# Performance work log

Measured on AMD Instinct MI355X. Metric: run time of the kernel, lower is better.

The kernel has to match this reference:

```python
import jax, jax.numpy as jnp
import numpy as np

LN_EPS = 1e-5
BN_EPS = 1e-5
HEADS = 8
KERNEL = 31
GROUP_SIZE = 8  # depthwise_conv groups = inner_dim // 8


def _ln(x, g, b):
    mu = jnp.mean(x, axis=-1, keepdims=True)
    var = jnp.var(x, axis=-1, keepdims=True)
    return (x - mu) * jax.lax.rsqrt(var + LN_EPS) * g + b


def _ff(x, g, b, w_in, b_in, w_out, b_out):
    h = _ln(x, g, b)
    y = h @ w_in.T + b_in
    a, c = jnp.split(y, 2, axis=-1)
    return (jax.nn.silu(a) * c) @ w_out.T + b_out


def _attn(x, g, b, wqkv, bqkv, wo, bo):
    B, S, _ = x.shape
    h = _ln(x, g, b)
    qkv = (h @ wqkv.T + bqkv).reshape(B, S, 3, HEADS, -1).transpose(2, 0, 3, 1, 4)
    q, k, v = qkv[0], qkv[1], qkv[2]  # [B,H,S,D]
    scale = q.shape[-1] ** -0.5
    scores = jnp.einsum('bhqd,bhkd->bhqk', q, k) * scale
    w = jax.nn.softmax(scores, axis=-1)
    o = jnp.einsum('bhqk,bhkd->bhqd', w, v)
    o = o.transpose(0, 2, 1, 3).reshape(B, S, -1)
    return o @ wo.T + bo


def _conv(x, g, b, pw1_w, pw1_b, dw_w, dw_b, bn_g, bn_b, bn_m, bn_v, pw2_w, pw2_b):
    h = _ln(x, g, b).transpose(0, 2, 1)  # [B, C, S]
    y = jnp.einsum('oc,bcs->bos', pw1_w[:, :, 0], h) + pw1_b[:, None]
    a, c = jnp.split(y, 2, axis=1)
    y = a * jax.nn.sigmoid(c)  # GLU over channel dim -> [B, inner, S]
    pad = (KERNEL - 1) // 2
    groups = y.shape[1] // dw_w.shape[1]  # inner_dim // 8
    y = jax.lax.conv_general_dilated(
        y, dw_w, window_strides=(1,), padding=[(pad, pad)],
        dimension_numbers=('NCH', 'OIH', 'NCH'), feature_group_count=groups)
    y = y + dw_b[:, None]
    y = (y - bn_m[:, None]) * jax.lax.rsqrt(bn_v[:, None] + BN_EPS) * bn_g[:, None] + bn_b[:, None]
    y = jax.nn.silu(y)
    y = jnp.einsum('oc,bcs->bos', pw2_w[:, :, 0], y) + pw2_b[:, None]
    return y.transpose(0, 2, 1)


def setup_inputs() -> dict:
    key = jax.random.key(0)
    dim, mult, exp = 512, 4, 2
    inner = dim * exp  # 1024
    ks = jax.random.split(key, 16)
    n = lambda k, shp: (jax.random.normal(k, shp, dtype=jnp.float32) * 0.02)
    d = {}
    d['x'] = jax.random.normal(ks[0], (8, 1024, dim), dtype=jnp.float32)
    # ff1
    d['ff1_g'] = jnp.ones((dim,), jnp.float32); d['ff1_b'] = jnp.zeros((dim,), jnp.float32)
    d['ff1_win'] = n(ks[1], (dim * mult * 2, dim)); d['ff1_bin'] = jnp.zeros((dim * mult * 2,), jnp.float32)
    d['ff1_wout'] = n(ks[2], (dim, dim * mult)); d['ff1_bout'] = jnp.zeros((dim,), jnp.float32)
    # attn
    d['attn_g'] = jnp.ones((dim,), jnp.float32); d['attn_b'] = jnp.zeros((dim,), jnp.float32)
    d['wqkv'] = n(ks[3], (3 * dim, dim)); d['bqkv'] = jnp.zeros((3 * dim,), jnp.float32)
    d['wo'] = n(ks[4], (dim, dim)); d['bo'] = jnp.zeros((dim,), jnp.float32)
    # conv
    d['conv_g'] = jnp.ones((dim,), jnp.float32); d['conv_b'] = jnp.zeros((dim,), jnp.float32)
    d['pw1_w'] = n(ks[5], (inner * 2, dim, 1)); d['pw1_b'] = jnp.zeros((inner * 2,), jnp.float32)
    d['dw_w'] = n(ks[6], (inner, GROUP_SIZE, KERNEL)); d['dw_b'] = jnp.zeros((inner,), jnp.float32)
    d['bn_g'] = jnp.ones((inner,), jnp.float32); d['bn_b'] = jnp.zeros((inner,), jnp.float32)
    d['bn_m'] = jnp.zeros((inner,), jnp.float32); d['bn_v'] = jnp.ones((inner,), jnp.float32)
    d['pw2_w'] = n(ks[7], (dim, inner, 1)); d['pw2_b'] = jnp.zeros((dim,), jnp.float32)
    # ff2
    d['ff2_g'] = jnp.ones((dim,), jnp.float32); d['ff2_b'] = jnp.zeros((dim,), jnp.float32)
    d['ff2_win'] = n(ks[8], (dim * mult * 2, dim)); d['ff2_bin'] = jnp.zeros((dim * mult * 2,), jnp.float32)
    d['ff2_wout'] = n(ks[9], (dim, dim * mult)); d['ff2_bout'] = jnp.zeros((dim,), jnp.float32)
    # final norm
    d['fn_g'] = jnp.ones((dim,), jnp.float32); d['fn_b'] = jnp.zeros((dim,), jnp.float32)
    return d


def reference(x, ff1_g, ff1_b, ff1_win, ff1_bin, ff1_wout, ff1_bout,
              attn_g, attn_b, wqkv, bqkv, wo, bo,
              conv_g, conv_b, pw1_w, pw1_b, dw_w, dw_b, bn_g, bn_b, bn_m, bn_v, pw2_w, pw2_b,
              ff2_g, ff2_b, ff2_win, ff2_bin, ff2_wout, ff2_bout, fn_g, fn_b):
    x = x + 0.5 * _ff(x, ff1_g, ff1_b, ff1_win, ff1_bin, ff1_wout, ff1_bout)
    x = x + _attn(x, attn_g, attn_b, wqkv, bqkv, wo, bo)
    x = x + _conv(x, conv_g, conv_b, pw1_w, pw1_b, dw_w, dw_b, bn_g, bn_b, bn_m, bn_v, pw2_w, pw2_b)
    x = x + 0.5 * _ff(x, ff2_g, ff2_b, ff2_win, ff2_bin, ff2_wout, ff2_bout)
    return _ln(x, fn_g, fn_b)
```

## Files before the change

kernel.cpp:

```cpp
#include <hip/hip_runtime.h>

#define SEQ   1024
#define BATCH 8
#define DIM   512
#define NTOK  (SEQ * BATCH)

typedef unsigned short ushort_t;
typedef unsigned int uint_t;
typedef __attribute__((ext_vector_type(8))) short s16x8;
typedef __attribute__((ext_vector_type(4))) float f32x4;

union F4 { float4 v; float f[4]; };

__device__ __forceinline__ float sigmoid_f(float x) { return 1.0f / (1.0f + expf(-x)); }
__device__ __forceinline__ float silu_f(float x)    { return x * sigmoid_f(x); }

__device__ __forceinline__ ushort_t f2bf(float x) {
  uint_t u = __float_as_uint(x);
  return (ushort_t)((u + 0x7FFFu + ((u >> 16) & 1u)) >> 16);
}
__device__ __forceinline__ float bf2f(ushort_t h) {
  return __uint_as_float(((uint_t)h) << 16);
}

__device__ __forceinline__ void gload16(const void* g, void* l) {
  __builtin_amdgcn_global_load_lds(
      (const __attribute__((address_space(1))) void*)g,
      (__attribute__((address_space(3))) void*)l,
      16, 0, 0);
}

struct CastArgs {
  const float* src[8];
  ushort_t*    dst[8];
  int          cum8[8];
};

__global__ __launch_bounds__(256) void f2b_multi(CastArgs a, int total8)
{
  const int i = blockIdx.x * 256 + threadIdx.x;
  if (i >= total8) return;
  int s = 0;
  #pragma unroll
  for (int k = 1; k < 8; ++k) s += (i >= a.cum8[k]) ? 1 : 0;
  const int j = i - a.cum8[s];
  const float* src = a.src[s] + (size_t)j * 8;
  F4 x0, x1;
  x0.v = *(const float4*)(src);
  x1.v = *(const float4*)(src + 4);
  uint4 o;
  o.x = (uint_t)f2bf(x0.f[0]) | ((uint_t)f2bf(x0.f[1]) << 16);
  o.y = (uint_t)f2bf(x0.f[2]) | ((uint_t)f2bf(x0.f[3]) << 16);
  o.z = (uint_t)f2bf(x1.f[0]) | ((uint_t)f2bf(x1.f[1]) << 16);
  o.w = (uint_t)f2bf(x1.f[2]) | ((uint_t)f2bf(x1.f[3]) << 16);
  *(uint4*)(a.dst[s] + (size_t)j * 8) = o;
}

template <int BF>
__global__ __launch_bounds__(256) void ln512_kernel(
    const float* __restrict__ in, const float* __restrict__ g,
    const float* __restrict__ b, void* __restrict__ outv)
{
  const int row = blockIdx.x * 4 + (threadIdx.x >> 6);
  const int l   = threadIdx.x & 63;
  const float* rp = in + (size_t)row * DIM + l * 8;
  F4 v0, v1;
  v0.v = *(const float4*)(rp);
  v1.v = *(const float4*)(rp + 4);
  float sum = 0.f, sq = 0.f;
  #pragma unroll
  for (int j = 0; j < 4; ++j) { sum += v0.f[j] + v1.f[j];
                                sq  += v0.f[j]*v0.f[j] + v1.f[j]*v1.f[j]; }
  #pragma unroll
  for (int m = 32; m >= 1; m >>= 1) {
    sum += __shfl_xor(sum, m, 64);
    sq  += __shfl_xor(sq,  m, 64);
  }
  const float mu   = sum * (1.0f / DIM);
  const float var  = sq * (1.0f / DIM) - mu * mu;
  const float rinv = rsqrtf(var + 1e-5f);
  F4 g0, g1, b0, b1;
  g0.v = *(const float4*)(g + l * 8);     g1.v = *(const float4*)(g + l * 8 + 4);
  b0.v = *(const float4*)(b + l * 8);     b1.v = *(const float4*)(b + l * 8 + 4);
  float o[8];
  #pragma unroll
  for (int j = 0; j < 4; ++j) {
    o[j]     = (v0.f[j] - mu) * rinv * g0.f[j] + b0.f[j];
    o[4 + j] = (v1.f[j] - mu) * rinv * g1.f[j] + b1.f[j];
  }
  if (BF) {
    uint4 u;
    u.x = (uint_t)f2bf(o[0]) | ((uint_t)f2bf(o[1]) << 16);
    u.y = (uint_t)f2bf(o[2]) | ((uint_t)f2bf(o[3]) << 16);
    u.z = (uint_t)f2bf(o[4]) | ((uint_t)f2bf(o[5]) << 16);
    u.w = (uint_t)f2bf(o[6]) | ((uint_t)f2bf(o[7]) << 16);
    *(uint4*)((ushort_t*)outv + (size_t)row * DIM + l * 8) = u;
  } else {
    F4 w0, w1;
    #pragma unroll
    for (int j = 0; j < 4; ++j) { w0.f[j] = o[j]; w1.f[j] = o[4 + j]; }
    *(float4*)((float*)outv + (size_t)row * DIM + l * 8)     = w0.v;
    *(float4*)((float*)outv + (size_t)row * DIM + l * 8 + 4) = w1.v;
  }
}

template <int EPI>
__global__ __launch_bounds__(256) void gemm_bf16(
    const ushort_t* __restrict__ A, const ushort_t* __restrict__ W,
    const float* __restrict__ bias, float* __restrict__ out,
    int N, int K, const float* __restrict__ res, float alpha)
{
  __shared__ ushort_t As[128 * 32];
  __shared__ ushort_t Ws[128 * 32];
  const int t    = threadIdx.x;
  const int lane = t & 63;
  const int w    = t >> 6;
  const int wm   = w >> 1, wn = w & 1;
  const int m0   = blockIdx.y << 7, n0 = blockIdx.x << 7;

  f32x4 acc[4][4] = {};

  const int lds0 = __builtin_amdgcn_readfirstlane((w * 64) * 16);
  const int lds1 = __builtin_amdgcn_readfirstlane((256 + w * 64) * 16);
  const int r0c  = t >> 2;
  const int r1c  = 64 + (t >> 2);
  const int cc   = (t & 3) << 3;

  for (int k0 = 0; k0 < K; k0 += 32) {
    gload16(A + (size_t)(m0 + r0c) * K + k0 + cc, (char*)As + lds0);
    gload16(A + (size_t)(m0 + r1c) * K + k0 + cc, (char*)As + lds1);
    gload16(W + (size_t)(n0 + r0c) * K + k0 + cc, (char*)Ws + lds0);
    gload16(W + (size_t)(n0 + r1c) * K + k0 + cc, (char*)Ws + lds1);
    __syncthreads();
    s16x8 a[4], b[4];
    #pragma unroll
    for (int i = 0; i < 4; ++i)
      a[i] = *(const s16x8*)&As[(wm * 64 + i * 16 + (lane & 15)) * 32 + ((lane >> 4) << 3)];
    #pragma unroll
    for (int j = 0; j < 4; ++j)
      b[j] = *(const s16x8*)&Ws[(wn * 64 + j * 16 + (lane & 15)) * 32 + ((lane >> 4) << 3)];
    #pragma unroll
    for (int i = 0; i < 4; ++i)
      #pragma unroll
      for (int j = 0; j < 4; ++j)
        acc[i][j] = __builtin_amdgcn_mfma_f32_16x16x32_bf16(a[i], b[j], acc[i][j], 0, 0, 0);
    __syncthreads();
  }

  #pragma unroll
  for (int i = 0; i < 4; ++i) {
    #pragma unroll
    for (int j = 0; j < 4; ++j) {
      const int col  = n0 + wn * 64 + j * 16 + (lane & 15);
      const int rowb = m0 + wm * 64 + i * 16 + ((lane >> 4) << 2);
      const float bc = bias[col];
      #pragma unroll
      for (int r = 0; r < 4; ++r) {
        const size_t idx = (size_t)(rowb + r) * N + col;
        float v = acc[i][j][r] + bc;
        if (EPI == 1) v = res[idx] + alpha * v;
        out[idx] = v;
      }
    }
  }
}

__global__ __launch_bounds__(256) void gemm_qkv_bf16(
    const ushort_t* __restrict__ A, const ushort_t* __restrict__ W,
    const float* __restrict__ bias, ushort_t* __restrict__ qkvb,
    ushort_t* __restrict__ Vt, int K)
{
  const int N = 1536;
  __shared__ ushort_t As[128 * 32];
  __shared__ ushort_t Ws[128 * 32];
  const int t    = threadIdx.x;
  const int lane = t & 63;
  const int w    = t >> 6;
  const int wm   = w >> 1, wn = w & 1;
  const int m0   = blockIdx.y << 7, n0 = blockIdx.x << 7;

  f32x4 acc[4][4] = {};

  const int lds0 = __builtin_amdgcn_readfirstlane((w * 64) * 16);
  const int lds1 = __builtin_amdgcn_readfirstlane((256 + w * 64) * 16);
  const int r0c  = t >> 2;
  const int r1c  = 64 + (t >> 2);
  const int cc   = (t & 3) << 3;

  for (int k0 = 0; k0 < K; k0 += 32) {
    gload16(A + (size_t)(m0 + r0c) * K + k0 + cc, (char*)As + lds0);
    gload16(A + (size_t)(m0 + r1c) * K + k0 + cc, (char*)As + lds1);
    gload16(W + (size_t)(n0 + r0c) * K + k0 + cc, (char*)Ws + lds0);
    gload16(W + (size_t)(n0 + r1c) * K + k0 + cc, (char*)Ws + lds1);
    __syncthreads();
    s16x8 a[4], b[4];
    #pragma unroll
    for (int i = 0; i < 4; ++i)
      a[i] = *(const s16x8*)&As[(wm * 64 + i * 16 + (lane & 15)) * 32 + ((lane >> 4) << 3)];
    #pragma unroll
    for (int j = 0; j < 4; ++j)
      b[j] = *(const s16x8*)&Ws[(wn * 64 + j * 16 + (lane & 15)) * 32 + ((lane >> 4) << 3)];
    #pragma unroll
    for (int i = 0; i < 4; ++i)
      #pragma unroll
      for (int j = 0; j < 4; ++j)
        acc[i][j] = __builtin_amdgcn_mfma_f32_16x16x32_bf16(a[i], b[j], acc[i][j], 0, 0, 0);
    __syncthreads();
  }

  #pragma unroll
  for (int i = 0; i < 4; ++i) {
    #pragma unroll
    for (int j = 0; j < 4; ++j) {
      const int col  = n0 + wn * 64 + j * 16 + (lane & 15);
      const int rowb = m0 + wm * 64 + i * 16 + ((lane >> 4) << 2);
      const float bc = bias[col];
      if (col < 1024) {
        #pragma unroll
        for (int r = 0; r < 4; ++r)
          qkvb[(size_t)(rowb + r) * N + col] = f2bf(acc[i][j][r] + bc);
      } else {
        const int vc = col - 1024;
        const int hh = vc >> 6, d = vc & 63;
        const int bb = rowb >> 10, s = rowb & 1023;
        ushort4 o;
        o.x = f2bf(acc[i][j][0] + bc);
        o.y = f2bf(acc[i][j][1] + bc);
        o.z = f2bf(acc[i][j][2] + bc);
        o.w = f2bf(acc[i][j][3] + bc);
        *(ushort4*)&Vt[(size_t)((bb * 8 + hh) * 64 + d) * 1024 + s] = o;
      }
    }
  }
}

template <int CGLU>
__global__ __launch_bounds__(256) void gemm_glu_bf16(
    const ushort_t* __restrict__ A, const ushort_t* __restrict__ W,
    const float* __restrict__ bias, ushort_t* __restrict__ out,
    int NG, int K)
{
  __shared__ ushort_t As[128 * 32];
  __shared__ ushort_t Was[64 * 32];
  __shared__ ushort_t Wcs[64 * 32];
  const int t    = threadIdx.x;
  const int lane = t & 63;
  const int w    = t >> 6;
  const int wm   = w >> 1, wn = w & 1;
  const int m0   = blockIdx.y << 7, n0 = blockIdx.x << 6;

  f32x4 acca[4][2] = {};
  f32x4 accc[4][2] = {};

  const int lds0 = __builtin_amdgcn_readfirstlane((w * 64) * 16);
  const int lds1 = __builtin_amdgcn_readfirstlane((256 + w * 64) * 16);
  const int r0c  = t >> 2;
  const int r1c  = 64 + (t >> 2);
  const int cc   = (t & 3) << 3;

  const ushort_t* Wc = W + (size_t)NG * K;

  for (int k0 = 0; k0 < K; k0 += 32) {
    gload16(A  + (size_t)(m0 + r0c) * K + k0 + cc, (char*)As  + lds0);
    gload16(A  + (size_t)(m0 + r1c) * K + k0 + cc, (char*)As  + lds1);
    gload16(W  + (size_t)(n0 + r0c) * K + k0 + cc, (char*)Was + lds0);
    gload16(Wc + (size_t)(n0 + r0c) * K + k0 + cc, (char*)Wcs + lds0);
    __syncthreads();
    s16x8 a[4], ba[2], bc[2];
    #pragma unroll
    for (int i = 0; i < 4; ++i)
      a[i] = *(const s16x8*)&As[(wm * 64 + i * 16 + (lane & 15)) * 32 + ((lane >> 4) << 3)];
    #pragma unroll
    for (int j = 0; j < 2; ++j) {
      const int roff = (wn * 32 + j * 16 + (lane & 15)) * 32 + ((lane >> 4) << 3);
      ba[j] = *(const s16x8*)&Was[roff];
      bc[j] = *(const s16x8*)&Wcs[roff];
    }
    #pragma unroll
    for (int i = 0; i < 4; ++i)
      #pragma unroll
      for (int j = 0; j < 2; ++j) {
        acca[i][j] = __builtin_amdgcn_mfma_f32_16x16x32_bf16(a[i], ba[j], acca[i][j], 0, 0, 0);
        accc[i][j] = __builtin_amdgcn_mfma_f32_16x16x32_bf16(a[i], bc[j], accc[i][j], 0, 0, 0);
      }
    __syncthreads();
  }

  #pragma unroll
  for (int i = 0; i < 4; ++i) {
    #pragma unroll
    for (int j = 0; j < 2; ++j) {
      const int col  = n0 + wn * 32 + j * 16 + (lane & 15);
      const int rowb = m0 + wm * 64 + i * 16 + ((lane >> 4) << 2);
      const float b1 = bias[col];
      const float b2 = bias[NG + col];
      #pragma unroll
      for (int r = 0; r < 4; ++r) {
        const float av = acca[i][j][r] + b1;
        const float cv = accc[i][j][r] + b2;
        const float o  = CGLU ? (av * sigmoid_f(cv)) : (silu_f(av) * cv);
        out[(size_t)(rowb + r) * NG + col] = f2bf(o);
      }
    }
  }
}

__global__ __launch_bounds__(256) void attn_mfma(
    const ushort_t* __restrict__ qkv, const ushort_t* __restrict__ Vt,
    ushort_t* __restrict__ out)
{
  __shared__ ushort_t Ks[64 * 64];
  __shared__ ushort_t Vs[64 * 64];
  __shared__ ushort_t Ps[4][16 * 64];

  const int t    = threadIdx.x;
  const int lane = t & 63;
  const int w    = t >> 6;
  const int i    = lane & 15;
  const int g    = lane >> 4;
  const int bh   = blockIdx.x;
  const int b    = bh >> 3, h = bh & 7;
  const int qt   = blockIdx.y;

  s16x8 qf[2];
  {
    const ushort_t* qrow = qkv + (size_t)(b * SEQ + qt * 64 + w * 16 + i) * 1536 + h * 64;
    qf[0] = *(const s16x8*)(qrow + g * 8);
    qf[1] = *(const s16x8*)(qrow + 32 + g * 8);
  }

  float m_[4], l_[4];
  f32x4 po[4] = {};
  #pragma unroll
  for (int r = 0; r < 4; ++r) { m_[r] = -1e30f; l_[r] = 0.0f; }

  const int e0   = w * 2;
  const int off0 = __builtin_amdgcn_readfirstlane(e0 * 1024);
  const int off1 = __builtin_amdgcn_readfirstlane(e0 * 1024 + 1024);

  for (int kvt = 0; kvt < 16; ++kvt) {
    __syncthreads();
    {
      const int s_a = e0 * 64 + lane;
      const int ra = s_a >> 3, ca = (s_a & 7) ^ (ra & 7);
      const int s_b = s_a + 64;
      const int rb = s_b >> 3, cb2 = (s_b & 7) ^ (rb & 7);
      gload16(qkv + (size_t)(b * SEQ + kvt * 64 + ra) * 1536 + 512 + h * 64 + ca * 8,
              (char*)Ks + off0);
      gload16(qkv + (size_t)(b * SEQ + kvt * 64 + rb) * 1536 + 512 + h * 64 + cb2 * 8,
              (char*)Ks + off1);
      gload16(Vt + (size_t)(bh * 64 + ra) * SEQ + kvt * 64 + ca * 8,
              (char*)Vs + off0);
      gload16(Vt + (size_t)(bh * 64 + rb) * SEQ + kvt * 64 + cb2 * 8,
              (char*)Vs + off1);
    }
    __syncthreads();

    f32x4 sc[4] = {};
    #pragma unroll
    for (int jj = 0; jj < 4; ++jj) {
      const int row = jj * 16 + i;
      #pragma unroll
      for (int dd = 0; dd < 2; ++dd) {
        const int byteoff = row * 128 + ((dd * 64 + g * 16) ^ ((row & 7) << 4));
        const s16x8 kf = *(const s16x8*)((const char*)Ks + byteoff);
        sc[jj] = __builtin_amdgcn_mfma_f32_16x16x32_bf16(qf[dd], kf, sc[jj], 0, 0, 0);
      }
    }

    #pragma unroll
    for (int r = 0; r < 4; ++r) {
      float v0 = sc[0][r] * 0.125f, v1 = sc[1][r] * 0.125f;
      float v2 = sc[2][r] * 0.125f, v3 = sc[3][r] * 0.125f;
      float mx = fmaxf(fmaxf(v0, v1), fmaxf(v2, v3));
      mx = fmaxf(mx, __shfl_xor(mx, 1));
      mx = fmaxf(mx, __shfl_xor(mx, 2));
      mx = fmaxf(mx, __shfl_xor(mx, 4));
      mx = fmaxf(mx, __shfl_xor(mx, 8));
      const float mn = fmaxf(m_[r], mx);
      const float al = __expf(m_[r] - mn);
      const float p0 = __expf(v0 - mn), p1 = __expf(v1 - mn);
      const float p2 = __expf(v2 - mn), p3 = __expf(v3 - mn);
      float rs = p0 + p1 + p2 + p3;
      rs += __shfl_xor(rs, 1); rs += __shfl_xor(rs, 2);
      rs += __shfl_xor(rs, 4); rs += __shfl_xor(rs, 8);
      l_[r] = l_[r] * al + rs;
      m_[r] = mn;
      #pragma unroll
      for (int dt = 0; dt < 4; ++dt) po[dt][r] *= al;
      const int q = 4 * g + r;
      const int key = (q & 7) << 4;
      ushort_t* pb = &Ps[w][0];
      ((ushort_t*)((char*)pb + q * 128 + ((2 * i) ^ key)))[0]       = f2bf(p0);
      ((ushort_t*)((char*)pb + q * 128 + ((32 + 2 * i) ^ key)))[0]  = f2bf(p1);
      ((ushort_t*)((char*)pb + q * 128 + ((64 + 2 * i) ^ key)))[0]  = f2bf(p2);
      ((ushort_t*)((char*)pb + q * 128 + ((96 + 2 * i) ^ key)))[0]  = f2bf(p3);
    }

    #pragma unroll
    for (int kc = 0; kc < 2; ++kc) {
      const int pbyte = i * 128 + ((kc * 64 + g * 16) ^ ((i & 7) << 4));
      const s16x8 pf = *(const s16x8*)((const char*)&Ps[w][0] + pbyte);
      #pragma unroll
      for (int dt = 0; dt < 4; ++dt) {
        const int vrow = dt * 16 + i;
        const int vbyte = vrow * 128 + ((kc * 64 + g * 16) ^ ((vrow & 7) << 4));
        const s16x8 vf = *(const s16x8*)((const char*)Vs + vbyte);
        po[dt] = __builtin_amdgcn_mfma_f32_16x16x32_bf16(pf, vf, po[dt], 0, 0, 0);
      }
    }
  }

  #pragma unroll
  for (int r = 0; r < 4; ++r) {
    const float inv = 1.0f / l_[r];
    const size_t row = (size_t)(b * SEQ + qt * 64 + w * 16 + 4 * g + r);
    #pragma unroll
    for (int dt = 0; dt < 4; ++dt)
      out[row * 512 + h * 64 + dt * 16 + i] = f2bf(po[dt][r] * inv);
  }
}

__global__ __launch_bounds__(256) void dwconv_kernel(
    const ushort_t* __restrict__ in, const float* __restrict__ w,
    const float* __restrict__ dwb, const float* __restrict__ bng,
    const float* __restrict__ bnb, const float* __restrict__ bnm,
    const float* __restrict__ bnv, ushort_t* __restrict__ out)
{
  __shared__ float tile[94][65];
  const int s0 = blockIdx.x << 6;
  const int c0 = blockIdx.y << 6;
  const int b  = blockIdx.z;
  const int t  = threadIdx.x;

  {
    const int cl4 = (t & 15) << 2;
    #pragma unroll
    for (int it = 0; it < 6; ++it) {
      const int rr = it * 16 + (t >> 4);
      if (rr < 94) {
        const int gs = s0 - 15 + rr;
        float4 fv = make_float4(0.f, 0.f, 0.f, 0.f);
        if (gs >= 0 && gs < SEQ) {
          ushort4 uv = *(const ushort4*)(in + (size_t)(b * SEQ + gs) * 1024 + c0 + cl4);
          fv = make_float4(bf2f(uv.x), bf2f(uv.y), bf2f(uv.z), bf2f(uv.w));
        }
        tile[rr][cl4 + 0] = fv.x;
        tile[rr][cl4 + 1] = fv.y;
        tile[rr][cl4 + 2] = fv.z;
        tile[rr][cl4 + 3] = fv.w;
      }
    }
  }
  __syncthreads();

  const int wv   = t >> 6;
  const int lane = t & 63;

  float res[16];
  #pragma unroll
  for (int grp = 0; grp < 2; ++grp) {
    const int chb = wv * 16 + grp * 8;
    const int gcb = __builtin_amdgcn_readfirstlane(c0 + chb);
    const float* wbase = w + (size_t)gcb * 248;
    float acc[8] = {};
    for (int ci = 0; ci < 8; ++ci) {
      float win[31];
      #pragma unroll
      for (int r = 0; r < 31; ++r) win[r] = tile[lane + r][chb + ci];
      const float* wp = wbase + ci * 31;
      #pragma unroll
      for (int co = 0; co < 8; ++co) {
        #pragma unroll
        for (int tap = 0; tap < 31; ++tap)
          acc[co] = fmaf(wp[co * 248 + tap], win[tap], acc[co]);
      }
    }
    #pragma unroll
    for (int co = 0; co < 8; ++co) res[grp * 8 + co] = acc[co];
  }

  __syncthreads();
  #pragma unroll
  for (int grp = 0; grp < 2; ++grp) {
    const int chb = wv * 16 + grp * 8;
    const int gcb = __builtin_amdgcn_readfirstlane(c0 + chb);
    #pragma unroll
    for (int co = 0; co < 8; ++co) {
      const int gc = gcb + co;
      float y = res[grp * 8 + co] + dwb[gc];
      y = (y - bnm[gc]) * rsqrtf(bnv[gc] + 1e-5f) * bng[gc] + bnb[gc];
      tile[lane][chb + co] = silu_f(y);
    }
  }
  __syncthreads();
  {
    const int r  = t >> 2;
    const int cq = (t & 3) << 4;
    uint4 o1;
    uint_t p[8];
    #pragma unroll
    for (int j = 0; j < 8; ++j) {
      const float a = tile[r][cq + 2 * j];
      const float c = tile[r][cq + 2 * j + 1];
      p[j] = (uint_t)f2bf(a) | ((uint_t)f2bf(c) << 16);
    }
    ushort_t* dst = out + (size_t)(b * SEQ + s0 + r) * 1024 + c0 + cq;
    o1 = make_uint4(p[0], p[1], p[2], p[3]);
    *(uint4*)dst = o1;
    o1 = make_uint4(p[4], p[5], p[6], p[7]);
    *(uint4*)(dst + 8) = o1;
  }
}

extern "C" void kernel_launch(void* const* d_in, const int* in_sizes, int n_in,
                              void* d_out, int out_size, void* d_ws, size_t ws_size,
                              hipStream_t stream)
{
  (void)in_sizes; (void)n_in; (void)out_size; (void)ws_size;
  const float* x        = (const float*)d_in[0];
  const float* ff1_g    = (const float*)d_in[1];
  const float* ff1_b    = (const float*)d_in[2];
  const float* ff1_win  = (const float*)d_in[3];
  const float* ff1_bin  = (const float*)d_in[4];
  const float* ff1_wout = (const float*)d_in[5];
  const float* ff1_bout = (const float*)d_in[6];
  const float* attn_g   = (const float*)d_in[7];
  const float* attn_b   = (const float*)d_in[8];
  const float* wqkv     = (const float*)d_in[9];
  const float* bqkv     = (const float*)d_in[10];
  const float* wo       = (const float*)d_in[11];
  const float* bo       = (const float*)d_in[12];
  const float* conv_g   = (const float*)d_in[13];
  const float* conv_b   = (const float*)d_in[14];
  const float* pw1_w    = (const float*)d_in[15];
  const float* pw1_b    = (const float*)d_in[16];
  const float* dw_w     = (const float*)d_in[17];
  const float* dw_b     = (const float*)d_in[18];
  const float* bn_g     = (const float*)d_in[19];
  const float* bn_b     = (const float*)d_in[20];
  const float* bn_m     = (const float*)d_in[21];
  const float* bn_v     = (const float*)d_in[22];
  const float* pw2_w    = (const float*)d_in[23];
  const float* pw2_b    = (const float*)d_in[24];
  const float* ff2_g    = (const float*)d_in[25];
  const float* ff2_b    = (const float*)d_in[26];
  const float* ff2_win  = (const float*)d_in[27];
  const float* ff2_bin  = (const float*)d_in[28];
  const float* ff2_wout = (const float*)d_in[29];
  const float* ff2_bout = (const float*)d_in[30];
  const float* fn_g     = (const float*)d_in[31];
  const float* fn_b     = (const float*)d_in[32];

  char* wsb = (char*)d_ws;
  float*    xc    = (float*)(wsb);
  ushort_t* qkvb  = (ushort_t*)(wsb + (size_t)(16 << 20));
  ushort_t* vtb   = (ushort_t*)(wsb + (size_t)(40 << 20));
  ushort_t* h_bf  = (ushort_t*)(wsb + (size_t)(48 << 20));
  ushort_t* g_bf  = (ushort_t*)(wsb + (size_t)(56 << 20));
  ushort_t* tb_bf = (ushort_t*)(wsb + (size_t)(88 << 20));
  ushort_t* cv_bf = (ushort_t*)(wsb + (size_t)(96 << 20));
  ushort_t* wb    = (ushort_t*)(wsb + (size_t)(112 << 20));

  ushort_t* ff1win_b  = wb;
  ushort_t* ff1wout_b = ff1win_b + 4096 * 512;
  ushort_t* wqkv_b    = ff1wout_b + 512 * 2048;
  ushort_t* wo_b      = wqkv_b + 1536 * 512;
  ushort_t* pw1w_b    = wo_b + 512 * 512;
  ushort_t* pw2w_b    = pw1w_b + 2048 * 512;
  ushort_t* ff2win_b  = pw2w_b + 512 * 1024;
  ushort_t* ff2wout_b = ff2win_b + 4096 * 512;

  float* outp = (float*)d_out;
  const dim3 B256(256);

  {
    CastArgs a;
    const float* srcs[8] = {ff1_win, ff1_wout, wqkv, wo, pw1_w, pw2_w, ff2_win, ff2_wout};
    ushort_t*    dsts[8] = {ff1win_b, ff1wout_b, wqkv_b, wo_b, pw1w_b, pw2w_b, ff2win_b, ff2wout_b};
    const int    ns[8]   = {4096*512, 512*2048, 1536*512, 512*512,
                            2048*512, 512*1024, 4096*512, 512*2048};
    int cum = 0;
    for (int i = 0; i < 8; ++i) {
      a.src[i] = srcs[i]; a.dst[i] = dsts[i]; a.cum8[i] = cum; cum += ns[i] / 8;
    }
    f2b_multi<<<dim3((cum + 255) / 256), B256, 0, stream>>>(a, cum);
  }

  ln512_kernel<1><<<dim3(NTOK / 4), B256, 0, stream>>>(x, ff1_g, ff1_b, h_bf);
  gemm_glu_bf16<0><<<dim3(32, 64), B256, 0, stream>>>(h_bf, ff1win_b, ff1_bin, g_bf, 2048, 512);
  gemm_bf16<1><<<dim3(4, 64), B256, 0, stream>>>(g_bf, ff1wout_b, ff1_bout, xc, 512, 2048, x, 0.5f);

  ln512_kernel<1><<<dim3(NTOK / 4), B256, 0, stream>>>(xc, attn_g, attn_b, h_bf);
  gemm_qkv_bf16<<<dim3(12, 64), B256, 0, stream>>>(h_bf, wqkv_b, bqkv, qkvb, vtb, 512);
  attn_mfma<<<dim3(64, 16), B256, 0, stream>>>(qkvb, vtb, tb_bf);
  gemm_bf16<1><<<dim3(4, 64), B256, 0, stream>>>(tb_bf, wo_b, bo, xc, 512, 512, xc, 1.0f);

  ln512_kernel<1><<<dim3(NTOK / 4), B256, 0, stream>>>(xc, conv_g, conv_b, h_bf);
  gemm_glu_bf16<1><<<dim3(16, 64), B256, 0, stream>>>(h_bf, pw1w_b, pw1_b, g_bf, 1024, 512);
  dwconv_kernel<<<dim3(16, 16, 8), B256, 0, stream>>>(g_bf, dw_w, dw_b, bn_g, bn_b, bn_m, bn_v, cv_bf);
  gemm_bf16<1><<<dim3(4, 64), B256, 0, stream>>>(cv_bf, pw2w_b, pw2_b, xc, 512, 1024, xc, 1.0f);

  ln512_kernel<1><<<dim3(NTOK / 4), B256, 0, stream>>>(xc, ff2_g, ff2_b, h_bf);
  gemm_glu_bf16<0><<<dim3(32, 64), B256, 0, stream>>>(h_bf, ff2win_b, ff2_bin, g_bf, 2048, 512);
  gemm_bf16<1><<<dim3(4, 64), B256, 0, stream>>>(g_bf, ff2wout_b, ff2_bout, xc, 512, 2048, xc, 0.5f);

  ln512_kernel<0><<<dim3(NTOK / 4), B256, 0, stream>>>(xc, fn_g, fn_b, outp);
}
```

Before: 671.2 us.

## Remap depthwise conv threads to channel-per-lane with register sliding window

Rewrites the grouped depthwise convolution so each lane owns one output channel and 16 consecutive sequence positions. Each input value loaded from shared memory is reused across up to 16 accumulators in a sliding window instead of reloading 31 taps per output. Weights are now per-lane vector loads rather than wave-uniform scalar loads. The output-staging pass through shared memory is dropped, and each lane writes scattered 2-byte bf16 stores straight to global memory. The shared tile loses its padding column and is filled with float4 stores.

```diff
diff --git a/kernel.cpp b/kernel.cpp
--- a/kernel.cpp
+++ b/kernel.cpp
@@ -427,7 +427,7 @@
     const float* __restrict__ bnb, const float* __restrict__ bnm,
     const float* __restrict__ bnv, ushort_t* __restrict__ out)
 {
-  __shared__ float tile[94][65];
+  __shared__ __align__(16) float tile[94][64];
   const int s0 = blockIdx.x << 6;
   const int c0 = blockIdx.y << 6;
   const int b  = blockIdx.z;
@@ -445,71 +445,45 @@
           ushort4 uv = *(const ushort4*)(in + (size_t)(b * SEQ + gs) * 1024 + c0 + cl4);
           fv = make_float4(bf2f(uv.x), bf2f(uv.y), bf2f(uv.z), bf2f(uv.w));
         }
-        tile[rr][cl4 + 0] = fv.x;
-        tile[rr][cl4 + 1] = fv.y;
-        tile[rr][cl4 + 2] = fv.z;
-        tile[rr][cl4 + 3] = fv.w;
+        *(float4*)&tile[rr][cl4] = fv;
       }
     }
   }
   __syncthreads();
 
-  const int wv   = t >> 6;
-  const int lane = t & 63;
-
-  float res[16];
-  #pragma unroll
-  for (int grp = 0; grp < 2; ++grp) {
-    const int chb = wv * 16 + grp * 8;
-    const int gcb = __builtin_amdgcn_readfirstlane(c0 + chb);
-    const float* wbase = w + (size_t)gcb * 248;
-    float acc[8] = {};
-    for (int ci = 0; ci < 8; ++ci) {
-      float win[31];
-      #pragma unroll
-      for (int r = 0; r < 31; ++r) win[r] = tile[lane + r][chb + ci];
-      const float* wp = wbase + ci * 31;
-      #pragma unroll
-      for (int co = 0; co < 8; ++co) {
-        #pragma unroll
-        for (int tap = 0; tap < 31; ++tap)
-          acc[co] = fmaf(wp[co * 248 + tap], win[tap], acc[co]);
-      }
-    }
-    #pragma unroll
-    for (int co = 0; co < 8; ++co) res[grp * 8 + co] = acc[co];
-  }
-
-  __syncthreads();
-  #pragma unroll
-  for (int grp = 0; grp < 2; ++grp) {
-    const int chb = wv * 16 + grp * 8;
-    const int gcb = __builtin_amdgcn_readfirstlane(c0 + chb);
-    #pragma unroll
-    for (int co = 0; co < 8; ++co) {
-      const int gc = gcb + co;
-      float y = res[grp * 8 + co] + dwb[gc];
-      y = (y - bnm[gc]) * rsqrtf(bnv[gc] + 1e-5f) * bng[gc] + bnb[gc];
-      tile[lane][chb + co] = silu_f(y);
-    }
-  }
-  __syncthreads();
-  {
-    const int r  = t >> 2;
-    const int cq = (t & 3) << 4;
-    uint4 o1;
-    uint_t p[8];
-    #pragma unroll
-    for (int j = 0; j < 8; ++j) {
-      const float a = tile[r][cq + 2 * j];
-      const float c = tile[r][cq + 2 * j + 1];
-      p[j] = (uint_t)f2bf(a) | ((uint_t)f2bf(c) << 16);
-    }
-    ushort_t* dst = out + (size_t)(b * SEQ + s0 + r) * 1024 + c0 + cq;
-    o1 = make_uint4(p[0], p[1], p[2], p[3]);
-    *(uint4*)dst = o1;
-    o1 = make_uint4(p[4], p[5], p[6], p[7]);
-    *(uint4*)(dst + 8) = o1;
+  const int c  = t & 63;
+  const int sb = (t >> 6) << 4;
+  const int gc = c0 + c;
+
+  float acc[16] = {};
+  const float* wc = w + (size_t)gc * 248;
+  for (int ci = 0; ci < 8; ++ci) {
+    const int cl = (c & 56) | ci;
+    const float* wp = wc + ci * 31;
+    float wt[31];
+    #pragma unroll
+    for (int a = 0; a < 46; ++a) {
+      const float va = tile[sb + a][cl];
+      if (a < 31) wt[a] = wp[a];
+      #pragma unroll
+      for (int j = 0; j < 16; ++j) {
+        if (j <= a && a - j <= 30)
+          acc[j] = fmaf(wt[a - j], va, acc[j]);
+      }
+    }
+  }
+
+  const float bias = dwb[gc];
+  const float mean = bnm[gc];
+  const float rstd = rsqrtf(bnv[gc] + 1e-5f);
+  const float gg   = bng[gc];
+  const float bb2  = bnb[gc];
+  #pragma unroll
+  for (int j = 0; j < 16; ++j) {
+    const int s = s0 + sb + j;
+    float y = acc[j] + bias;
+    y = (y - mean) * rstd * gg + bb2;
+    out[(size_t)(b * SEQ + s) * 1024 + gc] = f2bf(silu_f(y));
   }
 }
 
```

After: 615.9 us. -8.2%, faster.
